# Kernel optimization log

Measured on AMD Instinct MI355X. Metric: run time of the kernel, lower is better.

Reference implementation:

```python
import jax, jax.numpy as jnp
import numpy as np

B, S, D, H = 2, 2048, 1024, 16
HD = D // H  # head_dim = 64


def setup_inputs() -> dict:
    key = jax.random.key(0)
    ks = jax.random.split(key, 12)
    s = 1.0 / np.sqrt(D)
    inp = {
        "query": jax.random.normal(ks[0], (B, S, D), jnp.float32),
        "key": jax.random.normal(ks[1], (B, S, D), jnp.float32),
        "value": jax.random.normal(ks[2], (B, S, D), jnp.float32),
        # causal mask, shape (B, S, S); 0 means masked
        "mask": jnp.broadcast_to(jnp.tril(jnp.ones((S, S), jnp.int32)), (B, S, S)),
        "Wq": jax.random.normal(ks[3], (D, D), jnp.float32) * s,
        "bq": jnp.zeros((D,), jnp.float32),
        "Wk": jax.random.normal(ks[4], (D, D), jnp.float32) * s,
        "bk": jnp.zeros((D,), jnp.float32),
        "Wv": jax.random.normal(ks[5], (D, D), jnp.float32) * s,
        "bv": jnp.zeros((D,), jnp.float32),
        "Wo": jax.random.normal(ks[6], (D, D), jnp.float32) * s,
        "bo": jnp.zeros((D,), jnp.float32),
    }
    return inp


def reference(query, key, value, mask, Wq, bq, Wk, bk, Wv, bv, Wo, bo):
    # QKV projections (nn.Linear: x @ W.T + b), split into heads -> (B, H, S, HD)
    def proj(x, W, b):
        return (x @ W.T + b).reshape(B, S, H, HD).transpose(0, 2, 1, 3)

    q = proj(query, Wq, bq)
    k = proj(key, Wk, bk)
    v = proj(value, Wv, bv)

    # scores: (B, H, S, S)
    scores = jnp.einsum("bhqd,bhkd->bhqk", q, k) / np.sqrt(HD).astype(np.float32)
    scores = jnp.where(mask[:, None, :, :] == 0, jnp.float32(-1e9), scores)
    attn = jax.nn.softmax(scores, axis=-1)
    # dropout is identity in eval mode
    ctx = jnp.einsum("bhqk,bhkd->bhqd", attn, v)  # (B, H, S, HD)
    ctx = ctx.transpose(0, 2, 1, 3).reshape(B, S, D)
    return ctx @ Wo.T + bo
```

## Files before the change

### kernel.cpp

```cpp
#include <hip/hip_runtime.h>
#include <hip/hip_bf16.h>
#include <stdint.h>


#define LOG2E 1.4426950408889634f

typedef __bf16 bf16x8 __attribute__((ext_vector_type(8)));
typedef float f32x4 __attribute__((ext_vector_type(4)));

__device__ __forceinline__ ushort f2bf(float f) {
  union { float f; uint32_t u; } v; v.f = f;
  uint32_t u = v.u + 0x7FFFu + ((v.u >> 16) & 1u);
  return (ushort)(u >> 16);
}
__device__ __forceinline__ uint32_t pack2(float a, float b) {
  return (uint32_t)f2bf(a) | ((uint32_t)f2bf(b) << 16);
}
__device__ __forceinline__ uint32_t pack2t(float a, float b) {
  uint32_t ua = __builtin_bit_cast(uint32_t, a);
  uint32_t ub = __builtin_bit_cast(uint32_t, b);
  return (ua >> 16) | (ub & 0xFFFF0000u);
}
__device__ __forceinline__ bf16x8 ld_frag(const ushort* p) {
  return __builtin_bit_cast(bf16x8, *(const uint4*)p);
}
__device__ __forceinline__ void gl_lds16(const void* g, void* l) {
  __builtin_amdgcn_global_load_lds(
      (const __attribute__((address_space(1))) void*)g,
      (__attribute__((address_space(3))) void*)l, 16, 0, 0);
}

template <int ROWS>
__device__ __forceinline__ void stage_tile(const ushort* src, int stride,
                                           ushort* dst, int wid, int lane) {
  const int rloc = lane >> 3;
  const int gsrc = (lane & 7) ^ (rloc & 7);
  constexpr int RW = ROWS / 4;
  const ushort* s = src + (size_t)(wid * RW + rloc) * stride + gsrc * 8;
#pragma unroll
  for (int j = 0; j < RW / 8; ++j)
    gl_lds16(s + (size_t)(j * 8) * stride, dst + (wid * RW + j * 8) * 64);
}
__device__ __forceinline__ int swz(int row, int gran) {
  return row * 64 + ((gran ^ (row & 7)) << 3);
}

__global__ void cvt_all(const float* __restrict__ s0, const float* __restrict__ s1,
                        const float* __restrict__ s2, const float* __restrict__ s3,
                        const float* __restrict__ s4, const float* __restrict__ s5,
                        const float* __restrict__ s6, ushort* __restrict__ d0,
                        ushort* __restrict__ d1, ushort* __restrict__ d2,
                        ushort* __restrict__ d3, ushort* __restrict__ d4,
                        ushort* __restrict__ d5, ushort* __restrict__ d6) {
  const int M4 = 4096 * 1024, M1 = 1024 * 1024;
  const int total = (3 * M4 + 4 * M1) / 8;
  for (int u = blockIdx.x * 256 + threadIdx.x; u < total; u += gridDim.x * 256) {
    int i = u * 8;
    const float* s; ushort* d; int off;
    if (i < 3 * M4) {
      int y = i / M4; off = i - y * M4;
      s = (y == 0) ? s0 : (y == 1) ? s1 : s2;
      d = (y == 0) ? d0 : (y == 1) ? d1 : d2;
    } else {
      int j = i - 3 * M4;
      int y = j / M1; off = j - y * M1;
      s = (y == 0) ? s3 : (y == 1) ? s4 : (y == 2) ? s5 : s6;
      d = (y == 0) ? d3 : (y == 1) ? d4 : (y == 2) ? d5 : d6;
    }
    float4 f0 = ((const float4*)(s + off))[0];
    float4 f1 = ((const float4*)(s + off))[1];
    uint4 h;
    h.x = pack2(f0.x, f0.y); h.y = pack2(f0.z, f0.w);
    h.z = pack2(f1.x, f1.y); h.w = pack2(f1.z, f1.w);
    *(uint4*)(d + off) = h;
  }
}

template <int BN, int NX, bool OUT_BF16, bool PROJ3>
__global__ __launch_bounds__(256, 2) void gemm_bt(
    const ushort* __restrict__ A0, const ushort* __restrict__ A1, const ushort* __restrict__ A2,
    const ushort* __restrict__ W0, const ushort* __restrict__ W1, const ushort* __restrict__ W2,
    const float* __restrict__ b0, const float* __restrict__ b1, const float* __restrict__ b2,
    void* __restrict__ Y0, void* __restrict__ Y1, void* __restrict__ Y2,
    int Ndim, int Kdim) {
  __shared__ ushort Al[2][128 * 64];
  __shared__ ushort Bl[2][BN * 64];

  const int z = PROJ3 ? blockIdx.y : 0;
  const ushort* A = (z == 0) ? A0 : (z == 1) ? A1 : A2;
  const ushort* W = (z == 0) ? W0 : (z == 1) ? W1 : W2;
  const float* bias = (z == 0) ? b0 : (z == 1) ? b1 : b2;
  void* Yp = (z == 0) ? Y0 : (z == 1) ? Y1 : Y2;

  const int id = blockIdx.x;
  const int m = id & 7;
  const int s = id >> 3;
  const int by = m * 4 + (s & 3);
  const int bx = s >> 2;

  const int tid = threadIdx.x;
  const int wid = tid >> 6, lane = tid & 63;
  const int row0 = by * 128, col0 = bx * BN;
  const int wr = wid >> 1, wc = wid & 1;
  const int lr = lane & 15, lg = lane >> 4;
  constexpr int NF = BN / 32;

  const ushort* Arow = A + (size_t)row0 * Kdim;
  const ushort* Wrow = W + (size_t)col0 * Kdim;

  f32x4 acc[4][NF] = {};

  stage_tile<128>(Arow, Kdim, Al[0], wid, lane);
  stage_tile<BN>(Wrow, Kdim, Bl[0], wid, lane);
  __syncthreads();

  int cur = 0;
  for (int k0 = 0; k0 < Kdim; k0 += 64) {
    if (k0 + 64 < Kdim) {
      stage_tile<128>(Arow + k0 + 64, Kdim, Al[cur ^ 1], wid, lane);
      stage_tile<BN>(Wrow + k0 + 64, Kdim, Bl[cur ^ 1], wid, lane);
    }
    const ushort* Ac = Al[cur];
    const ushort* Bc = Bl[cur];
#pragma unroll
    for (int kk = 0; kk < 2; ++kk) {
      bf16x8 af[4], bfr[NF];
#pragma unroll
      for (int mm = 0; mm < 4; ++mm)
        af[mm] = ld_frag(&Ac[swz(wr * 64 + mm * 16 + lr, kk * 4 + lg)]);
#pragma unroll
      for (int n = 0; n < NF; ++n)
        bfr[n] = ld_frag(&Bc[swz(wc * (BN / 2) + n * 16 + lr, kk * 4 + lg)]);
#pragma unroll
      for (int mm = 0; mm < 4; ++mm)
#pragma unroll
        for (int n = 0; n < NF; ++n)
          acc[mm][n] = __builtin_amdgcn_mfma_f32_16x16x32_bf16(af[mm], bfr[n], acc[mm][n], 0, 0, 0);
    }
    __syncthreads();
    cur ^= 1;
  }

#pragma unroll
  for (int n = 0; n < NF; ++n) {
    int col = col0 + wc * (BN / 2) + n * 16 + lr;
    float bv = bias[col];
#pragma unroll
    for (int mm = 0; mm < 4; ++mm) {
#pragma unroll
      for (int r = 0; r < 4; ++r) {
        int row = row0 + wr * 64 + mm * 16 + lg * 4 + r;
        float v = acc[mm][n][r] + bv;
        if (OUT_BF16)
          ((ushort*)Yp)[(size_t)row * Ndim + col] = f2bf(v);
        else
          ((float*)Yp)[(size_t)row * Ndim + col] = v;
      }
    }
  }
}

__global__ __launch_bounds__(256, 2) void attn_kernel(
    const ushort* __restrict__ Qb, const ushort* __restrict__ Kb,
    const ushort* __restrict__ Vb, ushort* __restrict__ Cx) {
  __shared__ ushort Kl[2][64 * 64];
  __shared__ ushort Vt[64 * 64];
  __shared__ ushort Pl[4][16 * 64];

  const int tid = threadIdx.x;
  const int wid = tid >> 6, lane = tid & 63;
  const int lr = lane & 15, lg = lane >> 4;
  const int x = blockIdx.x;
  const int p = blockIdx.y;
  const int b = x >> 4, h = x & 15;
  const size_t base = (size_t)b * 2048 * 1024 + h * 64;
  const float SCL = 0.125f * LOG2E;
  const int vp = tid & 31;
  const int vc = tid >> 5;

#pragma unroll 1
  for (int seg = 0; seg < 2; ++seg) {
    const int qi = seg ? (31 - p) : p;
    const int qb0 = qi * 64;
    const int q0w = qb0 + wid * 16;
    const int nt = qi + 1;

    bf16x8 qf[2];
    {
      const ushort* qs = Qb + base + (size_t)(q0w + lr) * 1024 + lg * 8;
      qf[0] = ld_frag(qs);
      qf[1] = ld_frag(qs + 32);
    }

    f32x4 O[4] = {};
    float m_reg = -1e30f, l_reg = 0.f;

    stage_tile<64>(Kb + base, 1024, Kl[0], wid, lane);
    uint4 va = *(const uint4*)(Vb + base + (size_t)(2 * vp) * 1024 + vc * 8);
    uint4 vb = *(const uint4*)(Vb + base + (size_t)(2 * vp + 1) * 1024 + vc * 8);

#pragma unroll 1
    for (int t = 0; t < nt; ++t) {
      const int kv0 = t * 64;
      {
        const ushort* pA = (const ushort*)&va;
        const ushort* pB = (const ushort*)&vb;
#pragma unroll
        for (int j = 0; j < 8; ++j) {
          int d = vc * 8 + j;
          int idx = d * 64 + (((vp >> 2) ^ j) << 3) + ((vp * 2) & 7);
          *(uint32_t*)&Vt[idx] = (uint32_t)pA[j] | ((uint32_t)pB[j] << 16);
        }
      }
      __syncthreads();

      if (t + 1 < nt) {
        stage_tile<64>(Kb + base + (size_t)(kv0 + 64) * 1024, 1024, Kl[(t + 1) & 1], wid, lane);
        va = *(const uint4*)(Vb + base + (size_t)(kv0 + 64 + 2 * vp) * 1024 + vc * 8);
        vb = *(const uint4*)(Vb + base + (size_t)(kv0 + 64 + 2 * vp + 1) * 1024 + vc * 8);
      }

      const bool dm = (t == nt - 1);
      const ushort* Kc = Kl[t & 1];

      f32x4 st[4];
#pragma unroll
      for (int cb = 0; cb < 4; ++cb) {
        if (kv0 + cb * 16 > q0w + 15) {
          st[cb] = f32x4{-1e30f, -1e30f, -1e30f, -1e30f};
          continue;
        }
        f32x4 a = {};
#pragma unroll
        for (int kk = 0; kk < 2; ++kk) {
          bf16x8 kfrag = ld_frag(&Kc[swz(cb * 16 + lr, kk * 4 + lg)]);
          a = __builtin_amdgcn_mfma_f32_16x16x32_bf16(kfrag, qf[kk], a, 0, 0, 0);
        }
#pragma unroll
        for (int r = 0; r < 4; ++r) {
          float sv = a[r] * SCL;
          if (dm) {
            int kv = kv0 + cb * 16 + lg * 4 + r;
            if (kv > q0w + lr) sv = -1e30f;
          }
          a[r] = sv;
        }
        st[cb] = a;
      }

      float tmax = -1e30f;
#pragma unroll
      for (int cb = 0; cb < 4; ++cb) {
        float c01 = fmaxf(st[cb][0], st[cb][1]);
        float c23 = fmaxf(st[cb][2], st[cb][3]);
        tmax = fmaxf(tmax, fmaxf(c01, c23));
      }
      tmax = fmaxf(tmax, __shfl_xor(tmax, 16));
      tmax = fmaxf(tmax, __shfl_xor(tmax, 32));

      const bool skip = __all(tmax - m_reg <= 8.f);
      float mcur;
      if (skip) {
        mcur = m_reg;
      } else {
        mcur = fmaxf(m_reg, tmax);
        float alpha = exp2f(m_reg - mcur);
        m_reg = mcur;
        l_reg *= alpha;
        float aO[4];
#pragma unroll
        for (int r = 0; r < 4; ++r)
          aO[r] = __shfl(alpha, (lane & 48) | ((lane >> 2) & 12) | r);
#pragma unroll
        for (int n = 0; n < 4; ++n)
#pragma unroll
          for (int r = 0; r < 4; ++r) O[n][r] *= aO[r];
      }

      float ts = 0.f;
#pragma unroll
      for (int cb = 0; cb < 4; ++cb)
#pragma unroll
        for (int r = 0; r < 4; ++r) {
          float pv = exp2f(st[cb][r] - mcur);
          st[cb][r] = pv;
          ts += pv;
        }
      ts += __shfl_xor(ts, 16);
      ts += __shfl_xor(ts, 32);
      l_reg += ts;

      ushort* pw = &Pl[wid][0];
#pragma unroll
      for (int cb = 0; cb < 4; ++cb) {
        int g = ((cb * 2 + (lg >> 1)) ^ (lr & 7)) << 3;
        int idx = lr * 64 + g + ((lg & 1) * 4);
        *(uint32_t*)&pw[idx] = pack2t(st[cb][0], st[cb][1]);
        *(uint32_t*)&pw[idx + 2] = pack2t(st[cb][2], st[cb][3]);
      }

#pragma unroll
      for (int kk = 0; kk < 2; ++kk) {
        bf16x8 pa = ld_frag(&pw[swz(lr, kk * 4 + lg)]);
#pragma unroll
        for (int n = 0; n < 4; ++n) {
          bf16x8 vfr = ld_frag(&Vt[swz(n * 16 + lr, kk * 4 + lg)]);
          O[n] = __builtin_amdgcn_mfma_f32_16x16x32_bf16(pa, vfr, O[n], 0, 0, 0);
        }
      }
      __syncthreads();
    }

#pragma unroll
    for (int r = 0; r < 4; ++r) {
      float ls = __shfl(l_reg, (lane & 48) | ((lane >> 2) & 12) | r);
      float inv = 1.f / ls;
      size_t row = (size_t)b * 2048 + q0w + lg * 4 + r;
#pragma unroll
      for (int n = 0; n < 4; ++n)
        Cx[row * 1024 + h * 64 + n * 16 + lr] = f2bf(O[n][r] * inv);
    }
  }
}

extern "C" void kernel_launch(void* const* d_in, const int* in_sizes, int n_in,
                              void* d_out, int out_size, void* d_ws, size_t ws_size,
                              hipStream_t stream) {
  const float* query = (const float*)d_in[0];
  const float* key_i = (const float*)d_in[1];
  const float* value = (const float*)d_in[2];
  const float* Wq = (const float*)d_in[4];
  const float* bq = (const float*)d_in[5];
  const float* Wk = (const float*)d_in[6];
  const float* bk = (const float*)d_in[7];
  const float* Wv = (const float*)d_in[8];
  const float* bv = (const float*)d_in[9];
  const float* Wo = (const float*)d_in[10];
  const float* bo = (const float*)d_in[11];
  float* out = (float*)d_out;

  const size_t MD = (size_t)4096 * 1024;
  const size_t DD = (size_t)1024 * 1024;
  ushort* qbf = (ushort*)d_ws;
  ushort* kbf = qbf + MD;
  ushort* vbf = kbf + MD;
  ushort* Wqb = vbf + MD;
  ushort* Wkb = Wqb + DD;
  ushort* Wvb = Wkb + DD;
  ushort* Wob = Wvb + DD;
  ushort* Qb = Wob + DD;
  ushort* Kb = Qb + MD;
  ushort* Vb = Kb + MD;
  ushort* Cx = Vb + MD;

  cvt_all<<<2048, 256, 0, stream>>>(query, key_i, value, Wq, Wk, Wv, Wo,
                                    qbf, kbf, vbf, Wqb, Wkb, Wvb, Wob);

  gemm_bt<128, 8, true, true><<<dim3(256, 3), 256, 0, stream>>>(
      qbf, kbf, vbf, Wqb, Wkb, Wvb, bq, bk, bv, Qb, Kb, Vb, 1024, 1024);

  attn_kernel<<<dim3(32, 16), 256, 0, stream>>>(Qb, Kb, Vb, Cx);

  gemm_bt<64, 16, false, false><<<dim3(512, 1), 256, 0, stream>>>(
      Cx, Cx, Cx, Wob, Wob, Wob, bo, bo, bo, out, out, out, 1024, 1024);
}
```

Before: 262.7 us.

## Switch GEMMs to 8-wave single-buffer tiles and split attention KV across wave pairs

The GEMM kernels now use 512 threads (8 waves) with a single LDS buffer, a 2x4 wave grid and a plain 3D launch grid in place of the swizzled block order and double-buffered prefetch. The attention kernel shrinks query tiles to 32 rows and doubles the grid. Two wave pairs take alternating KV tiles, V tiles are double-buffered, and the two partial softmax states are merged through LDS at the end. The aim is more parallelism and occupancy in attention and wider GEMM blocks, at the cost of losing load/compute overlap in the GEMM and adding a merge step and idle waves per KV tile in attention.

New measurement: 275.6 us. +4.9%, slower.

```diff
diff --git a/kernel.cpp b/kernel.cpp
--- a/kernel.cpp
+++ b/kernel.cpp
@@ -4,6 +4,7 @@
 
 
 #define LOG2E 1.4426950408889634f
+#define BAR __builtin_amdgcn_s_barrier()
 
 typedef __bf16 bf16x8 __attribute__((ext_vector_type(8)));
 typedef float f32x4 __attribute__((ext_vector_type(4)));
@@ -30,19 +31,20 @@
       (__attribute__((address_space(3))) void*)l, 16, 0, 0);
 }
 
-template <int ROWS>
+__device__ __forceinline__ int swz(int row, int gran) {
+  return row * 64 + ((gran ^ (row & 7)) << 3);
+}
+
+template <int ROWS, int NW>
 __device__ __forceinline__ void stage_tile(const ushort* src, int stride,
                                            ushort* dst, int wid, int lane) {
   const int rloc = lane >> 3;
   const int gsrc = (lane & 7) ^ (rloc & 7);
-  constexpr int RW = ROWS / 4;
+  constexpr int RW = ROWS / NW;
   const ushort* s = src + (size_t)(wid * RW + rloc) * stride + gsrc * 8;
 #pragma unroll
   for (int j = 0; j < RW / 8; ++j)
     gl_lds16(s + (size_t)(j * 8) * stride, dst + (wid * RW + j * 8) * 64);
-}
-__device__ __forceinline__ int swz(int row, int gran) {
-  return row * 64 + ((gran ^ (row & 7)) << 3);
 }
 
 __global__ void cvt_all(const float* __restrict__ s0, const float* __restrict__ s1,
@@ -76,81 +78,69 @@
   }
 }
 
-template <int BN, int NX, bool OUT_BF16, bool PROJ3>
-__global__ __launch_bounds__(256, 2) void gemm_bt(
+template <int BN, bool OUT_BF16, bool PROJ3>
+__global__ __launch_bounds__(512, 2) void gemm8(
     const ushort* __restrict__ A0, const ushort* __restrict__ A1, const ushort* __restrict__ A2,
     const ushort* __restrict__ W0, const ushort* __restrict__ W1, const ushort* __restrict__ W2,
     const float* __restrict__ b0, const float* __restrict__ b1, const float* __restrict__ b2,
     void* __restrict__ Y0, void* __restrict__ Y1, void* __restrict__ Y2,
     int Ndim, int Kdim) {
-  __shared__ ushort Al[2][128 * 64];
-  __shared__ ushort Bl[2][BN * 64];
-
-  const int z = PROJ3 ? blockIdx.y : 0;
+  __shared__ ushort Al[128 * 64];
+  __shared__ ushort Bl[BN * 64];
+
+  const int z = PROJ3 ? blockIdx.z : 0;
   const ushort* A = (z == 0) ? A0 : (z == 1) ? A1 : A2;
   const ushort* W = (z == 0) ? W0 : (z == 1) ? W1 : W2;
   const float* bias = (z == 0) ? b0 : (z == 1) ? b1 : b2;
   void* Yp = (z == 0) ? Y0 : (z == 1) ? Y1 : Y2;
 
-  const int id = blockIdx.x;
-  const int m = id & 7;
-  const int s = id >> 3;
-  const int by = m * 4 + (s & 3);
-  const int bx = s >> 2;
-
   const int tid = threadIdx.x;
   const int wid = tid >> 6, lane = tid & 63;
-  const int row0 = by * 128, col0 = bx * BN;
-  const int wr = wid >> 1, wc = wid & 1;
+  const int row0 = blockIdx.y * 128, col0 = blockIdx.x * BN;
+  const int wr = wid >> 2, wc = wid & 3;
   const int lr = lane & 15, lg = lane >> 4;
-  constexpr int NF = BN / 32;
+  constexpr int NF = BN / 64;
+  constexpr int WC = BN / 4;
 
   const ushort* Arow = A + (size_t)row0 * Kdim;
   const ushort* Wrow = W + (size_t)col0 * Kdim;
 
   f32x4 acc[4][NF] = {};
 
-  stage_tile<128>(Arow, Kdim, Al[0], wid, lane);
-  stage_tile<BN>(Wrow, Kdim, Bl[0], wid, lane);
-  __syncthreads();
-
-  int cur = 0;
-  for (int k0 = 0; k0 < Kdim; k0 += 64) {
-    if (k0 + 64 < Kdim) {
-      stage_tile<128>(Arow + k0 + 64, Kdim, Al[cur ^ 1], wid, lane);
-      stage_tile<BN>(Wrow + k0 + 64, Kdim, Bl[cur ^ 1], wid, lane);
-    }
-    const ushort* Ac = Al[cur];
-    const ushort* Bc = Bl[cur];
+  const int NT = Kdim >> 6;
+#pragma unroll 1
+  for (int t = 0; t < NT; ++t) {
+    stage_tile<128, 8>(Arow + t * 64, Kdim, Al, wid, lane);
+    stage_tile<BN, 8>(Wrow + t * 64, Kdim, Bl, wid, lane);
+    __syncthreads();
 #pragma unroll
     for (int kk = 0; kk < 2; ++kk) {
-      bf16x8 af[4], bfr[NF];
-#pragma unroll
-      for (int mm = 0; mm < 4; ++mm)
-        af[mm] = ld_frag(&Ac[swz(wr * 64 + mm * 16 + lr, kk * 4 + lg)]);
+      bf16x8 af[4], bf[NF];
+#pragma unroll
+      for (int m = 0; m < 4; ++m)
+        af[m] = ld_frag(&Al[swz(wr * 64 + m * 16 + lr, kk * 4 + lg)]);
 #pragma unroll
       for (int n = 0; n < NF; ++n)
-        bfr[n] = ld_frag(&Bc[swz(wc * (BN / 2) + n * 16 + lr, kk * 4 + lg)]);
-#pragma unroll
-      for (int mm = 0; mm < 4; ++mm)
+        bf[n] = ld_frag(&Bl[swz(wc * WC + n * 16 + lr, kk * 4 + lg)]);
+#pragma unroll
+      for (int m = 0; m < 4; ++m)
 #pragma unroll
         for (int n = 0; n < NF; ++n)
-          acc[mm][n] = __builtin_amdgcn_mfma_f32_16x16x32_bf16(af[mm], bfr[n], acc[mm][n], 0, 0, 0);
+          acc[m][n] = __builtin_amdgcn_mfma_f32_16x16x32_bf16(af[m], bf[n], acc[m][n], 0, 0, 0);
     }
     __syncthreads();
-    cur ^= 1;
   }
 
 #pragma unroll
   for (int n = 0; n < NF; ++n) {
-    int col = col0 + wc * (BN / 2) + n * 16 + lr;
+    int col = col0 + wc * WC + n * 16 + lr;
     float bv = bias[col];
 #pragma unroll
-    for (int mm = 0; mm < 4; ++mm) {
+    for (int m = 0; m < 4; ++m) {
 #pragma unroll
       for (int r = 0; r < 4; ++r) {
-        int row = row0 + wr * 64 + mm * 16 + lg * 4 + r;
-        float v = acc[mm][n][r] + bv;
+        int row = row0 + wr * 64 + m * 16 + lg * 4 + r;
+        float v = acc[m][n][r] + bv;
         if (OUT_BF16)
           ((ushort*)Yp)[(size_t)row * Ndim + col] = f2bf(v);
         else
@@ -160,15 +150,16 @@
   }
 }
 
-__global__ __launch_bounds__(256, 2) void attn_kernel(
+__global__ __launch_bounds__(256, 4) void attn_kernel(
     const ushort* __restrict__ Qb, const ushort* __restrict__ Kb,
     const ushort* __restrict__ Vb, ushort* __restrict__ Cx) {
   __shared__ ushort Kl[2][64 * 64];
-  __shared__ ushort Vt[64 * 64];
+  __shared__ ushort Vt[2][64 * 64];
   __shared__ ushort Pl[4][16 * 64];
 
   const int tid = threadIdx.x;
   const int wid = tid >> 6, lane = tid & 63;
+  const int wq = wid & 1, wk = wid >> 1;
   const int lr = lane & 15, lg = lane >> 4;
   const int x = blockIdx.x;
   const int p = blockIdx.y;
@@ -180,10 +171,10 @@
 
 #pragma unroll 1
   for (int seg = 0; seg < 2; ++seg) {
-    const int qi = seg ? (31 - p) : p;
-    const int qb0 = qi * 64;
-    const int q0w = qb0 + wid * 16;
-    const int nt = qi + 1;
+    const int qi = seg ? (63 - p) : p;
+    const int qb0 = qi * 32;
+    const int q0w = qb0 + wq * 16;
+    const int nt = (qi >> 1) + 1;
 
     bf16x8 qf[2];
     {
@@ -195,7 +186,7 @@
     f32x4 O[4] = {};
     float m_reg = -1e30f, l_reg = 0.f;
 
-    stage_tile<64>(Kb + base, 1024, Kl[0], wid, lane);
+    stage_tile<64, 4>(Kb + base, 1024, Kl[0], wid, lane);
     uint4 va = *(const uint4*)(Vb + base + (size_t)(2 * vp) * 1024 + vc * 8);
     uint4 vb = *(const uint4*)(Vb + base + (size_t)(2 * vp + 1) * 1024 + vc * 8);
 
@@ -205,121 +196,156 @@
       {
         const ushort* pA = (const ushort*)&va;
         const ushort* pB = (const ushort*)&vb;
+        ushort* vt = Vt[t & 1];
 #pragma unroll
         for (int j = 0; j < 8; ++j) {
-          int d = vc * 8 + j;
-          int idx = d * 64 + (((vp >> 2) ^ j) << 3) + ((vp * 2) & 7);
-          *(uint32_t*)&Vt[idx] = (uint32_t)pA[j] | ((uint32_t)pB[j] << 16);
+          int idx = (vc * 8 + j) * 64 + (((vp >> 2) ^ j) << 3) + ((vp * 2) & 7);
+          *(uint32_t*)&vt[idx] = (uint32_t)pA[j] | ((uint32_t)pB[j] << 16);
         }
       }
       __syncthreads();
 
       if (t + 1 < nt) {
-        stage_tile<64>(Kb + base + (size_t)(kv0 + 64) * 1024, 1024, Kl[(t + 1) & 1], wid, lane);
+        stage_tile<64, 4>(Kb + base + (size_t)(kv0 + 64) * 1024, 1024,
+                          Kl[(t + 1) & 1], wid, lane);
         va = *(const uint4*)(Vb + base + (size_t)(kv0 + 64 + 2 * vp) * 1024 + vc * 8);
         vb = *(const uint4*)(Vb + base + (size_t)(kv0 + 64 + 2 * vp + 1) * 1024 + vc * 8);
       }
 
-      const bool dm = (t == nt - 1);
-      const ushort* Kc = Kl[t & 1];
-
-      f32x4 st[4];
-#pragma unroll
-      for (int cb = 0; cb < 4; ++cb) {
-        if (kv0 + cb * 16 > q0w + 15) {
-          st[cb] = f32x4{-1e30f, -1e30f, -1e30f, -1e30f};
-          continue;
-        }
-        f32x4 a = {};
+      if (wk == (t & 1)) {
+        const bool dm = (t == nt - 1);
+        const ushort* Kc = Kl[t & 1];
+
+        f32x4 st[4];
+#pragma unroll
+        for (int cb = 0; cb < 4; ++cb) {
+          if (kv0 + cb * 16 > q0w + 15) {
+            st[cb] = f32x4{-1e30f, -1e30f, -1e30f, -1e30f};
+            continue;
+          }
+          f32x4 a = {};
+#pragma unroll
+          for (int kk = 0; kk < 2; ++kk) {
+            bf16x8 kfrag = ld_frag(&Kc[swz(cb * 16 + lr, kk * 4 + lg)]);
+            a = __builtin_amdgcn_mfma_f32_16x16x32_bf16(kfrag, qf[kk], a, 0, 0, 0);
+          }
+#pragma unroll
+          for (int r = 0; r < 4; ++r) {
+            float sv = a[r] * SCL;
+            if (dm) {
+              int kv = kv0 + cb * 16 + lg * 4 + r;
+              if (kv > q0w + lr) sv = -1e30f;
+            }
+            a[r] = sv;
+          }
+          st[cb] = a;
+        }
+
+        float tmax = -1e30f;
+#pragma unroll
+        for (int cb = 0; cb < 4; ++cb) {
+          float c01 = fmaxf(st[cb][0], st[cb][1]);
+          float c23 = fmaxf(st[cb][2], st[cb][3]);
+          tmax = fmaxf(tmax, fmaxf(c01, c23));
+        }
+        tmax = fmaxf(tmax, __shfl_xor(tmax, 16));
+        tmax = fmaxf(tmax, __shfl_xor(tmax, 32));
+
+        const bool skip = __all(tmax - m_reg <= 8.f);
+        float mcur;
+        if (skip) {
+          mcur = m_reg;
+        } else {
+          mcur = fmaxf(m_reg, tmax);
+          float alpha = exp2f(m_reg - mcur);
+          m_reg = mcur;
+          l_reg *= alpha;
+          float aO[4];
+#pragma unroll
+          for (int r = 0; r < 4; ++r)
+            aO[r] = __shfl(alpha, (lane & 48) | ((lane >> 2) & 12) | r);
+#pragma unroll
+          for (int n = 0; n < 4; ++n)
+#pragma unroll
+            for (int r = 0; r < 4; ++r) O[n][r] *= aO[r];
+        }
+
+        float ts = 0.f;
+#pragma unroll
+        for (int cb = 0; cb < 4; ++cb)
+#pragma unroll
+          for (int r = 0; r < 4; ++r) {
+            float pv = exp2f(st[cb][r] - mcur);
+            st[cb][r] = pv;
+            ts += pv;
+          }
+        ts += __shfl_xor(ts, 16);
+        ts += __shfl_xor(ts, 32);
+        l_reg += ts;
+
+        ushort* pw = &Pl[wid][0];
+#pragma unroll
+        for (int cb = 0; cb < 4; ++cb) {
+          int g = ((cb * 2 + (lg >> 1)) ^ (lr & 7)) << 3;
+          int idx = lr * 64 + g + ((lg & 1) * 4);
+          *(uint32_t*)&pw[idx] = pack2t(st[cb][0], st[cb][1]);
+          *(uint32_t*)&pw[idx + 2] = pack2t(st[cb][2], st[cb][3]);
+        }
+
+        const ushort* vt = Vt[t & 1];
 #pragma unroll
         for (int kk = 0; kk < 2; ++kk) {
-          bf16x8 kfrag = ld_frag(&Kc[swz(cb * 16 + lr, kk * 4 + lg)]);
-          a = __builtin_amdgcn_mfma_f32_16x16x32_bf16(kfrag, qf[kk], a, 0, 0, 0);
-        }
-#pragma unroll
-        for (int r = 0; r < 4; ++r) {
-          float sv = a[r] * SCL;
-          if (dm) {
-            int kv = kv0 + cb * 16 + lg * 4 + r;
-            if (kv > q0w + lr) sv = -1e30f;
-          }
-          a[r] = sv;
-        }
-        st[cb] = a;
-      }
-
-      float tmax = -1e30f;
-#pragma unroll
-      for (int cb = 0; cb < 4; ++cb) {
-        float c01 = fmaxf(st[cb][0], st[cb][1]);
-        float c23 = fmaxf(st[cb][2], st[cb][3]);
-        tmax = fmaxf(tmax, fmaxf(c01, c23));
-      }
-      tmax = fmaxf(tmax, __shfl_xor(tmax, 16));
-      tmax = fmaxf(tmax, __shfl_xor(tmax, 32));
-
-      const bool skip = __all(tmax - m_reg <= 8.f);
-      float mcur;
-      if (skip) {
-        mcur = m_reg;
-      } else {
-        mcur = fmaxf(m_reg, tmax);
-        float alpha = exp2f(m_reg - mcur);
-        m_reg = mcur;
-        l_reg *= alpha;
-        float aO[4];
+          bf16x8 pa = ld_frag(&pw[swz(lr, kk * 4 + lg)]);
+#pragma unroll
+          for (int n = 0; n < 4; ++n) {
+            bf16x8 vfr = ld_frag(&vt[swz(n * 16 + lr, kk * 4 + lg)]);
+            O[n] = __builtin_amdgcn_mfma_f32_16x16x32_bf16(pa, vfr, O[n], 0, 0, 0);
+          }
+        }
+      }
+      __syncthreads();
+    }
+
+    float* mrg = (float*)&Kl[0][0];
+    float* mw = mrg + wq * 1088;
+    if (wk == 1) {
+#pragma unroll
+      for (int n = 0; n < 4; ++n)
 #pragma unroll
         for (int r = 0; r < 4; ++r)
-          aO[r] = __shfl(alpha, (lane & 48) | ((lane >> 2) & 12) | r);
-#pragma unroll
-        for (int n = 0; n < 4; ++n)
-#pragma unroll
-          for (int r = 0; r < 4; ++r) O[n][r] *= aO[r];
-      }
-
-      float ts = 0.f;
-#pragma unroll
-      for (int cb = 0; cb < 4; ++cb)
-#pragma unroll
-        for (int r = 0; r < 4; ++r) {
-          float pv = exp2f(st[cb][r] - mcur);
-          st[cb][r] = pv;
-          ts += pv;
-        }
-      ts += __shfl_xor(ts, 16);
-      ts += __shfl_xor(ts, 32);
-      l_reg += ts;
-
-      ushort* pw = &Pl[wid][0];
-#pragma unroll
-      for (int cb = 0; cb < 4; ++cb) {
-        int g = ((cb * 2 + (lg >> 1)) ^ (lr & 7)) << 3;
-        int idx = lr * 64 + g + ((lg & 1) * 4);
-        *(uint32_t*)&pw[idx] = pack2t(st[cb][0], st[cb][1]);
-        *(uint32_t*)&pw[idx + 2] = pack2t(st[cb][2], st[cb][3]);
-      }
-
-#pragma unroll
-      for (int kk = 0; kk < 2; ++kk) {
-        bf16x8 pa = ld_frag(&pw[swz(lr, kk * 4 + lg)]);
+          mw[(lg * 4 + r) * 64 + n * 16 + lr] = O[n][r];
+      if (lg == 0) {
+        mw[1024 + lr] = m_reg;
+        mw[1040 + lr] = l_reg;
+      }
+    }
+    __syncthreads();
+    if (wk == 0) {
+      float mB = mw[1024 + lr], lB = mw[1040 + lr];
+      float mS = fmaxf(m_reg, mB);
+      float alpha = exp2f(m_reg - mS), beta = exp2f(mB - mS);
+      float lS = l_reg * alpha + lB * beta;
+      float linv = 1.f / lS;
+      float aO[4], bO[4], iO[4];
+#pragma unroll
+      for (int r = 0; r < 4; ++r) {
+        int src = (lane & 48) | ((lane >> 2) & 12) | r;
+        aO[r] = __shfl(alpha, src);
+        bO[r] = __shfl(beta, src);
+        iO[r] = __shfl(linv, src);
+      }
+#pragma unroll
+      for (int r = 0; r < 4; ++r) {
+        size_t row = (size_t)b * 2048 + q0w + lg * 4 + r;
 #pragma unroll
         for (int n = 0; n < 4; ++n) {
-          bf16x8 vfr = ld_frag(&Vt[swz(n * 16 + lr, kk * 4 + lg)]);
-          O[n] = __builtin_amdgcn_mfma_f32_16x16x32_bf16(pa, vfr, O[n], 0, 0, 0);
-        }
-      }
-      __syncthreads();
-    }
-
-#pragma unroll
-    for (int r = 0; r < 4; ++r) {
-      float ls = __shfl(l_reg, (lane & 48) | ((lane >> 2) & 12) | r);
-      float inv = 1.f / ls;
-      size_t row = (size_t)b * 2048 + q0w + lg * 4 + r;
-#pragma unroll
-      for (int n = 0; n < 4; ++n)
-        Cx[row * 1024 + h * 64 + n * 16 + lr] = f2bf(O[n][r] * inv);
-    }
+          float ob = mw[(lg * 4 + r) * 64 + n * 16 + lr];
+          float val = (O[n][r] * aO[r] + ob * bO[r]) * iO[r];
+          Cx[row * 1024 + h * 64 + n * 16 + lr] = f2bf(val);
+        }
+      }
+    }
+    __syncthreads();
   }
 }
 
@@ -356,11 +382,11 @@
   cvt_all<<<2048, 256, 0, stream>>>(query, key_i, value, Wq, Wk, Wv, Wo,
                                     qbf, kbf, vbf, Wqb, Wkb, Wvb, Wob);
 
-  gemm_bt<128, 8, true, true><<<dim3(256, 3), 256, 0, stream>>>(
+  gemm8<128, true, true><<<dim3(8, 32, 3), 512, 0, stream>>>(
       qbf, kbf, vbf, Wqb, Wkb, Wvb, bq, bk, bv, Qb, Kb, Vb, 1024, 1024);
 
-  attn_kernel<<<dim3(32, 16), 256, 0, stream>>>(Qb, Kb, Vb, Cx);
-
-  gemm_bt<64, 16, false, false><<<dim3(512, 1), 256, 0, stream>>>(
+  attn_kernel<<<dim3(32, 32), 256, 0, stream>>>(Qb, Kb, Vb, Cx);
+
+  gemm8<64, false, false><<<dim3(16, 32, 1), 512, 0, stream>>>(
       Cx, Cx, Cx, Wob, Wob, Wob, bo, bo, bo, out, out, out, 1024, 1024);
 }
```
